# Kernel optimization log

Measured on AMD Instinct MI355X. Metric: run time of the kernel, lower is better.

Reference implementation:

```python
import jax, jax.numpy as jnp
import numpy as np

N_NODES = 100000
N_EDGES = 3200000
DROP_P = 0.5


def gcn_conv(x, W, b, src, dst, deg_inv_sqrt, n):
    # PyG GCNConv with self-loops already folded into (src, dst):
    # out[j] = sum_{(i->j)} dinv[i]*dinv[j] * (x W)[i] + b
    h = x @ W
    norm = deg_inv_sqrt[src] * deg_inv_sqrt[dst]          # [E+N]
    msg = h[src] * norm[:, None]                          # [E+N, d_out]
    out = jax.ops.segment_sum(msg, dst, num_segments=n)
    return out + b


def dropout(x, key, p=DROP_P):
    keep = jax.random.bernoulli(key, 1.0 - p, x.shape)
    return jnp.where(keep, x / (1.0 - p), 0.0)


def setup_inputs() -> dict:
    key = jax.random.key(0)
    ks = jax.random.split(key, 8)
    x = jax.random.normal(ks[0], (N_NODES, 64), dtype=jnp.float32)
    edge_index = jax.random.randint(ks[1], (2, N_EDGES), 0, N_NODES, dtype=jnp.int64)
    def glorot(k, fin, fout):
        lim = float(np.sqrt(6.0 / (fin + fout)))
        return jax.random.uniform(k, (fin, fout), jnp.float32, -lim, lim)
    return {
        "x": x,
        "edge_index": edge_index,
        "W1": glorot(ks[2], 64, 32), "b1": jnp.zeros((32,), jnp.float32),
        "W2": glorot(ks[3], 32, 64), "b2": jnp.zeros((64,), jnp.float32),
        "W3": glorot(ks[4], 64, 32), "b3": jnp.zeros((32,), jnp.float32),
    }


def reference(x, edge_index, W1, b1, W2, b2, W3, b3):
    n = x.shape[0]
    loops = jnp.arange(n, dtype=edge_index.dtype)
    src = jnp.concatenate([edge_index[0], loops])          # [E+N]
    dst = jnp.concatenate([edge_index[1], loops])
    deg = jax.ops.segment_sum(jnp.ones_like(dst, dtype=x.dtype), dst, num_segments=n)
    deg_inv_sqrt = jnp.where(deg > 0, jax.lax.rsqrt(deg), 0.0)

    dkey = jax.random.key(42)
    k1, k2 = jax.random.split(dkey)

    h = gcn_conv(x, W1, b1, src, dst, deg_inv_sqrt, n)
    h = jax.nn.celu(h)
    h = dropout(h, k1)
    h = gcn_conv(h, W2, b2, src, dst, deg_inv_sqrt, n)
    h = jax.nn.celu(h)
    h = dropout(h, k2)
    h = gcn_conv(h, W3, b3, src, dst, deg_inv_sqrt, n)
    return jax.nn.celu(h)
```

## Files before the change

kernel.cpp:

```cpp
#include <hip/hip_runtime.h>
#include <stdint.h>
#include <stddef.h>

typedef _Float16 half_t;
typedef _Float16 half4 __attribute__((ext_vector_type(4)));
typedef _Float16 half8 __attribute__((ext_vector_type(8)));

__host__ __device__ __forceinline__ uint32_t rotl32(uint32_t v, uint32_t r) {
  return (v << r) | (v >> (32u - r));
}

__host__ __device__ __forceinline__ void tf2x32(uint32_t k0, uint32_t k1,
                                                uint32_t x0, uint32_t x1,
                                                uint32_t& o0, uint32_t& o1) {
  uint32_t ks2 = k0 ^ k1 ^ 0x1BD11BDAu;
  x0 += k0; x1 += k1;
  x0 += x1; x1 = rotl32(x1, 13); x1 ^= x0;
  x0 += x1; x1 = rotl32(x1, 15); x1 ^= x0;
  x0 += x1; x1 = rotl32(x1, 26); x1 ^= x0;
  x0 += x1; x1 = rotl32(x1, 6);  x1 ^= x0;
  x0 += k1; x1 += ks2 + 1u;
  x0 += x1; x1 = rotl32(x1, 17); x1 ^= x0;
  x0 += x1; x1 = rotl32(x1, 29); x1 ^= x0;
  x0 += x1; x1 = rotl32(x1, 16); x1 ^= x0;
  x0 += x1; x1 = rotl32(x1, 24); x1 ^= x0;
  x0 += ks2; x1 += k0 + 2u;
  x0 += x1; x1 = rotl32(x1, 13); x1 ^= x0;
  x0 += x1; x1 = rotl32(x1, 15); x1 ^= x0;
  x0 += x1; x1 = rotl32(x1, 26); x1 ^= x0;
  x0 += x1; x1 = rotl32(x1, 6);  x1 ^= x0;
  x0 += k0; x1 += k1 + 3u;
  x0 += x1; x1 = rotl32(x1, 17); x1 ^= x0;
  x0 += x1; x1 = rotl32(x1, 29); x1 ^= x0;
  x0 += x1; x1 = rotl32(x1, 16); x1 ^= x0;
  x0 += x1; x1 = rotl32(x1, 24); x1 ^= x0;
  x0 += k1; x1 += ks2 + 4u;
  x0 += x1; x1 = rotl32(x1, 13); x1 ^= x0;
  x0 += x1; x1 = rotl32(x1, 15); x1 ^= x0;
  x0 += x1; x1 = rotl32(x1, 26); x1 ^= x0;
  x0 += x1; x1 = rotl32(x1, 6);  x1 ^= x0;
  x0 += ks2; x1 += k0 + 5u;
  o0 = x0; o1 = x1;
}

__device__ __forceinline__ bool tf_keep(uint32_t k0, uint32_t k1, uint32_t idx) {
  uint32_t o0, o1;
  tf2x32(k0, k1, 0u, idx, o0, o1);
  return ((o0 ^ o1) >> 31) == 0u;
}

#define CHUNK 4096
#define STASH 5120

__global__ __launch_bounds__(1024) void zero1024(uint32_t* __restrict__ p) {
  p[threadIdx.x] = 0u;
}

__global__ __launch_bounds__(1024) void k4_binhist(const int* __restrict__ src,
                                                   const int* __restrict__ dst,
                                                   uint32_t* __restrict__ tbl,
                                                   uint32_t* __restrict__ gbcnt,
                                                   uint32_t* __restrict__ staging,
                                                   int E, int NB) {
  __shared__ uint32_t lcur[1024];
  __shared__ uint32_t ls[1024];
  __shared__ uint32_t stage[CHUNK];
  int tid = threadIdx.x;
  lcur[tid] = 0u;
  __syncthreads();
  int base = blockIdx.x * CHUNK;
  int end = min(base + CHUNK, E);
  uint32_t dv[4], sv[4];
  int m = 0;
  for (int i = base + tid; i < end; i += 1024) {
    dv[m] = (uint32_t)dst[i];
    sv[m] = (uint32_t)src[i];
    ++m;
  }
  for (int q = 0; q < m; ++q) atomicAdd(&lcur[dv[q] >> 7], 1u);
  __syncthreads();
  uint32_t v = lcur[tid];
  ls[tid] = v;
  __syncthreads();
  for (int off = 1; off < 1024; off <<= 1) {
    uint32_t t = (tid >= off) ? ls[tid - off] : 0u;
    __syncthreads();
    if (tid >= off) ls[tid] += t;
    __syncthreads();
  }
  uint32_t excl = ls[tid] - v;
  if (tid < NB) {
    tbl[(size_t)blockIdx.x * NB + tid] = (excl << 16) | v;
    if (v) atomicAdd(&gbcnt[tid], v);
  }
  lcur[tid] = excl;
  __syncthreads();
  for (int q = 0; q < m; ++q) {
    uint32_t d = dv[q];
    uint32_t p = atomicAdd(&lcur[d >> 7], 1u);
    stage[p] = ((d & 127u) << 17) | sv[q];
  }
  __syncthreads();
  int cnt_total = end - base;
  uint32_t* outp = staging + (size_t)blockIdx.x * CHUNK;
  for (int i = tid; i < cnt_total; i += 1024) outp[i] = stage[i];
}

__global__ __launch_bounds__(1024) void k3_bscan(const uint32_t* __restrict__ gbcnt,
                                                 uint32_t* __restrict__ bbase, int NB) {
  __shared__ uint32_t s[1024];
  int i = threadIdx.x;
  uint32_t v = (i < NB) ? gbcnt[i] : 0u;
  s[i] = v;
  __syncthreads();
  for (int off = 1; off < 1024; off <<= 1) {
    uint32_t t = (i >= off) ? s[i - off] : 0u;
    __syncthreads();
    if (i >= off) s[i] += t;
    __syncthreads();
  }
  if (i < NB) bbase[i] = s[i] - v;
}

__global__ __launch_bounds__(1024) void k5_fin(
    const uint32_t* __restrict__ staging, const uint32_t* __restrict__ tbl,
    const uint32_t* __restrict__ bbase, uint32_t* __restrict__ rowp,
    float* __restrict__ dinv, uint32_t* __restrict__ esrc,
    int n, int E, int NBLK, int NB) {
  __shared__ uint32_t loff[1024];
  __shared__ uint32_t P[1025];
  __shared__ uint32_t ls[1024];
  __shared__ uint32_t stash[STASH];
  __shared__ uint32_t lc[128];
  __shared__ uint32_t sc[128];
  __shared__ uint32_t lcur[128];
  int tid = threadIdx.x;
  int b = blockIdx.x;
  if (tid < 128) lc[tid] = 0u;
  uint32_t packed = (tid < NBLK) ? tbl[(size_t)tid * NB + b] : 0u;
  uint32_t v = packed & 0xFFFFu;
  loff[tid] = packed >> 16;
  ls[tid] = v;
  __syncthreads();
  for (int off = 1; off < 1024; off <<= 1) {
    uint32_t t = (tid >= off) ? ls[tid - off] : 0u;
    __syncthreads();
    if (tid >= off) ls[tid] += t;
    __syncthreads();
  }
  P[tid] = ls[tid] - v;
  if (tid == 1023) P[1024] = ls[1023];
  __syncthreads();
  uint32_t total = P[NBLK];
  for (uint32_t q = (uint32_t)tid; q < total; q += 1024u) {
    int lo = 0, hi = NBLK;
    while (hi - lo > 1) {
      int mid = (lo + hi) >> 1;
      if (P[mid] <= q) lo = mid; else hi = mid;
    }
    uint32_t e = staging[(size_t)lo * CHUNK + loff[lo] + (q - P[lo])];
    if (q < (uint32_t)STASH) stash[q] = e;
    atomicAdd(&lc[e >> 17], 1u);
  }
  __syncthreads();
  uint32_t myc = (tid < 128) ? lc[tid] : 0u;
  if (tid < 128) sc[tid] = myc;
  __syncthreads();
  for (int off = 1; off < 128; off <<= 1) {
    uint32_t t = (tid < 128 && tid >= off) ? sc[tid - off] : 0u;
    __syncthreads();
    if (tid < 128 && tid >= off) sc[tid] += t;
    __syncthreads();
  }
  uint32_t s = bbase[b];
  if (tid < 128) {
    uint32_t gstart = s + sc[tid] - myc;
    int node = (b << 7) + tid;
    if (node < n) {
      rowp[node] = gstart;
      dinv[node] = 1.0f / sqrtf((float)(myc + 1u));
    }
    lcur[tid] = gstart;
  }
  if (b == 0 && tid == 0) rowp[n] = (uint32_t)E;
  __syncthreads();
  uint32_t lim = total < (uint32_t)STASH ? total : (uint32_t)STASH;
  for (uint32_t q = (uint32_t)tid; q < lim; q += 1024u) {
    uint32_t e = stash[q];
    uint32_t pos = atomicAdd(&lcur[e >> 17], 1u);
    esrc[pos] = e & 0x1FFFFu;
  }
  if (total > (uint32_t)STASH) {
    for (uint32_t q = (uint32_t)STASH + (uint32_t)tid; q < total; q += 1024u) {
      int lo = 0, hi = NBLK;
      while (hi - lo > 1) {
        int mid = (lo + hi) >> 1;
        if (P[mid] <= q) lo = mid; else hi = mid;
      }
      uint32_t e = staging[(size_t)lo * CHUNK + loff[lo] + (q - P[lo])];
      uint32_t pos = atomicAdd(&lcur[e >> 17], 1u);
      esrc[pos] = e & 0x1FFFFu;
    }
  }
}

__global__ __launch_bounds__(256) void gemm_n64_k32(
    const float* __restrict__ X, const float* __restrict__ W,
    const float* __restrict__ dinv, half_t* __restrict__ out16, int n) {
  __shared__ float Ws[64 * 32];
  __shared__ float Xs[32 * 68];
  int tid = threadIdx.x;
  {
    const float4* Wv = (const float4*)W;
    float4* Wsv = (float4*)Ws;
    Wsv[tid] = Wv[tid];
    Wsv[tid + 256] = Wv[tid + 256];
  }
  int row0 = blockIdx.x * 32;
  {
    const float4* Xv = (const float4*)(X + (size_t)row0 * 64);
    int lim = (n - row0) * 16;
    float4 z = make_float4(0.f, 0.f, 0.f, 0.f);
    int i0 = tid, i1 = tid + 256;
    float4 v0 = (i0 < lim) ? Xv[i0] : z;
    float4 v1 = (i1 < lim) ? Xv[i1] : z;
    *(float4*)(Xs + (i0 >> 4) * 68 + ((i0 & 15) << 2)) = v0;
    *(float4*)(Xs + (i1 >> 4) * 68 + ((i1 & 15) << 2)) = v1;
  }
  __syncthreads();
  int r = tid >> 3;
  int c4 = (tid & 7) << 2;
  int row = row0 + r;
  if (row >= n) return;
  float4 acc = make_float4(0.f, 0.f, 0.f, 0.f);
#pragma unroll
  for (int k = 0; k < 64; k += 4) {
    float4 xv = *(const float4*)(Xs + r * 68 + k);
    float4 w0 = *(const float4*)(Ws + (k + 0) * 32 + c4);
    float4 w1 = *(const float4*)(Ws + (k + 1) * 32 + c4);
    float4 w2 = *(const float4*)(Ws + (k + 2) * 32 + c4);
    float4 w3 = *(const float4*)(Ws + (k + 3) * 32 + c4);
    acc.x = fmaf(xv.x, w0.x, acc.x); acc.y = fmaf(xv.x, w0.y, acc.y);
    acc.z = fmaf(xv.x, w0.z, acc.z); acc.w = fmaf(xv.x, w0.w, acc.w);
    acc.x = fmaf(xv.y, w1.x, acc.x); acc.y = fmaf(xv.y, w1.y, acc.y);
    acc.z = fmaf(xv.y, w1.z, acc.z); acc.w = fmaf(xv.y, w1.w, acc.w);
    acc.x = fmaf(xv.z, w2.x, acc.x); acc.y = fmaf(xv.z, w2.y, acc.y);
    acc.z = fmaf(xv.z, w2.z, acc.z); acc.w = fmaf(xv.z, w2.w, acc.w);
    acc.x = fmaf(xv.w, w3.x, acc.x); acc.y = fmaf(xv.w, w3.y, acc.y);
    acc.z = fmaf(xv.w, w3.z, acc.z); acc.w = fmaf(xv.w, w3.w, acc.w);
  }
  float dj = dinv[row];
  half4 h;
  h.x = (half_t)(acc.x * dj); h.y = (half_t)(acc.y * dj);
  h.z = (half_t)(acc.z * dj); h.w = (half_t)(acc.w * dj);
  *(half4*)(out16 + (size_t)row * 32 + c4) = h;
}

__global__ __launch_bounds__(256) void gather_fin(
    const half_t* __restrict__ hs, const uint32_t* __restrict__ rowp,
    const uint32_t* __restrict__ esrc, const float* __restrict__ dinv,
    const float* __restrict__ bias, float* __restrict__ outf,
    half_t* __restrict__ outh, int n, int mode, uint32_t k0, uint32_t k1,
    float fone) {
  __shared__ __align__(16) float ldsred[256];
  (void)fone;
  int tid = threadIdx.x;
  int gt = blockIdx.x * 256 + tid;
  int j = gt >> 5;
  int g = tid >> 5;
  int l = tid & 31;
  int eslot = l >> 2;
  int chunk = l & 3;
  float acc[8] = {0.f, 0.f, 0.f, 0.f, 0.f, 0.f, 0.f, 0.f};
  uint32_t e0 = 0, deg = 0;
  float selfv = 0.f, dj = 0.f;
  if (j < n) {
    e0 = rowp[j];
    deg = rowp[j + 1] - e0;
    selfv = (float)hs[(size_t)j * 32 + l];
    dj = dinv[j];
  }
  const half_t* hp = hs + (size_t)(chunk << 3);
  const half8 hz = {(half_t)0, (half_t)0, (half_t)0, (half_t)0,
                    (half_t)0, (half_t)0, (half_t)0, (half_t)0};
  for (uint32_t base = 0; base < deg; base += 64u) {
    uint32_t rem = deg - base;
    if (rem > 64u) rem = 64u;
    uint32_t li0 = (uint32_t)l < rem ? (uint32_t)l : rem - 1u;
    uint32_t t1 = 32u + (uint32_t)l;
    uint32_t li1 = t1 < rem ? t1 : rem - 1u;
    uint32_t idx0 = __builtin_nontemporal_load(&esrc[e0 + base + li0]);
    uint32_t idx1 = __builtin_nontemporal_load(&esrc[e0 + base + li1]);
    half8 v0, v1, v2, v3, v4, v5, v6, v7;
#define GLOAD(KK, IDX, VOUT)                                              \
    {                                                                     \
      uint32_t kp = (uint32_t)(KK) + (uint32_t)eslot;                     \
      uint32_t s = (uint32_t)__shfl((int)(IDX), (int)(kp & 31u), 32);     \
      VOUT = hz;                                                          \
      if (kp < rem) VOUT = *(const half8*)(hp + ((size_t)s << 5));        \
    }
    GLOAD(0,  idx0, v0)
    GLOAD(8,  idx0, v1)
    GLOAD(16, idx0, v2)
    GLOAD(24, idx0, v3)
    GLOAD(32, idx1, v4)
    GLOAD(40, idx1, v5)
    GLOAD(48, idx1, v6)
    GLOAD(56, idx1, v7)
#undef GLOAD
    half8 s01 = v0 + v1;
    half8 s23 = v2 + v3;
    half8 s45 = v4 + v5;
    half8 s67 = v6 + v7;
#pragma unroll
    for (int q = 0; q < 8; ++q) {
      acc[q] += (float)s01[q];
      acc[q] += (float)s23[q];
      acc[q] += (float)s45[q];
      acc[q] += (float)s67[q];
    }
  }
#pragma unroll
  for (int m = 4; m <= 16; m <<= 1) {
#pragma unroll
    for (int q = 0; q < 8; ++q) acc[q] += __shfl_xor(acc[q], m);
  }
  if (l < 4) {
    *(float4*)(&ldsred[(g << 5) + (chunk << 3) + 0]) =
        make_float4(acc[0], acc[1], acc[2], acc[3]);
    *(float4*)(&ldsred[(g << 5) + (chunk << 3) + 4]) =
        make_float4(acc[4], acc[5], acc[6], acc[7]);
  }
  __builtin_amdgcn_wave_barrier();
  if (j >= n) return;
  float sum = ldsred[(g << 5) + l];
  sum += selfv;
  float v = dj * sum;
  if (mode == 1) {
    v += bias[l];
    v = v > 0.f ? v : expm1f(v);
    __builtin_nontemporal_store(v, &outf[gt]);
  } else if (mode == 3) {
    v += bias[l];
    v = v > 0.f ? v : expm1f(v);
    v = tf_keep(k0, k1, (uint32_t)gt) ? v * 2.f : 0.f;
    v *= dj;
    __builtin_nontemporal_store((half_t)v, &outh[gt]);
  } else {
    __builtin_nontemporal_store(v, &outf[gt]);
  }
}

__global__ __launch_bounds__(256) void gather_gemm2(
    const half_t* __restrict__ hs, const uint32_t* __restrict__ rowp,
    const uint32_t* __restrict__ esrc, const float* __restrict__ dinv,
    const float* __restrict__ W2, const float* __restrict__ b2,
    const float* __restrict__ W3, half_t* __restrict__ outh,
    int n, uint32_t k0, uint32_t k1) {
  __shared__ __align__(16) float ldsred[256];
  __shared__ __align__(16) float W2s[32 * 64];
  __shared__ __align__(16) float W3s[64 * 32];
  __shared__ __align__(16) float b2s[64];
  __shared__ __align__(16) float tls[8 * 64];
  int tid = threadIdx.x;
  {
    const float4* w2v = (const float4*)W2;
    const float4* w3v = (const float4*)W3;
    float4* s2 = (float4*)W2s;
    float4* s3 = (float4*)W3s;
    s2[tid] = w2v[tid];
    s2[tid + 256] = w2v[tid + 256];
    s3[tid] = w3v[tid];
    s3[tid + 256] = w3v[tid + 256];
    if (tid < 16) ((float4*)b2s)[tid] = ((const float4*)b2)[tid];
  }
  __syncthreads();
  int j = blockIdx.x * 8 + (tid >> 5);
  int g = tid >> 5;
  int l = tid & 31;
  int eslot = l >> 2;
  int chunk = l & 3;
  float acc[8] = {0.f, 0.f, 0.f, 0.f, 0.f, 0.f, 0.f, 0.f};
  uint32_t e0 = 0, deg = 0;
  float selfv = 0.f, dj = 0.f;
  if (j < n) {
    e0 = rowp[j];
    deg = rowp[j + 1] - e0;
    selfv = (float)hs[(size_t)j * 32 + l];
    dj = dinv[j];
  }
  const half_t* hp = hs + (size_t)(chunk << 3);
  const half8 hz = {(half_t)0, (half_t)0, (half_t)0, (half_t)0,
                    (half_t)0, (half_t)0, (half_t)0, (half_t)0};
  for (uint32_t base = 0; base < deg; base += 64u) {
    uint32_t rem = deg - base;
    if (rem > 64u) rem = 64u;
    uint32_t li0 = (uint32_t)l < rem ? (uint32_t)l : rem - 1u;
    uint32_t t1 = 32u + (uint32_t)l;
    uint32_t li1 = t1 < rem ? t1 : rem - 1u;
    uint32_t idx0 = __builtin_nontemporal_load(&esrc[e0 + base + li0]);
    uint32_t idx1 = __builtin_nontemporal_load(&esrc[e0 + base + li1]);
    half8 v0, v1, v2, v3, v4, v5, v6, v7;
#define GLOAD(KK, IDX, VOUT)                                              \
    {                                                                     \
      uint32_t kp = (uint32_t)(KK) + (uint32_t)eslot;                     \
      uint32_t s = (uint32_t)__shfl((int)(IDX), (int)(kp & 31u), 32);     \
      VOUT = hz;                                                          \
      if (kp < rem) VOUT = *(const half8*)(hp + ((size_t)s << 5));        \
    }
    GLOAD(0,  idx0, v0)
    GLOAD(8,  idx0, v1)
    GLOAD(16, idx0, v2)
    GLOAD(24, idx0, v3)
    GLOAD(32, idx1, v4)
    GLOAD(40, idx1, v5)
    GLOAD(48, idx1, v6)
    GLOAD(56, idx1, v7)
#undef GLOAD
    half8 s01 = v0 + v1;
    half8 s23 = v2 + v3;
    half8 s45 = v4 + v5;
    half8 s67 = v6 + v7;
#pragma unroll
    for (int q = 0; q < 8; ++q) {
      acc[q] += (float)s01[q];
      acc[q] += (float)s23[q];
      acc[q] += (float)s45[q];
      acc[q] += (float)s67[q];
    }
  }
#pragma unroll
  for (int m = 4; m <= 16; m <<= 1) {
#pragma unroll
    for (int q = 0; q < 8; ++q) acc[q] += __shfl_xor(acc[q], m);
  }
  if (l < 4) {
    *(float4*)(&ldsred[(g << 5) + (chunk << 3) + 0]) =
        make_float4(acc[0], acc[1], acc[2], acc[3]);
    *(float4*)(&ldsred[(g << 5) + (chunk << 3) + 4]) =
        make_float4(acc[4], acc[5], acc[6], acc[7]);
  }
  __builtin_amdgcn_wave_barrier();
  float hv = dj * (ldsred[(g << 5) + l] + selfv);
  __builtin_amdgcn_wave_barrier();
  ldsred[(g << 5) + l] = hv;
  __builtin_amdgcn_wave_barrier();
  int c0 = l << 1;
  float t0 = 0.f, t1v = 0.f;
#pragma unroll
  for (int k = 0; k < 32; ++k) {
    float xk = ldsred[(g << 5) + k];
    t0 = fmaf(xk, W2s[k * 64 + c0], t0);
    t1v = fmaf(xk, W2s[k * 64 + c0 + 1], t1v);
  }
  t0 += b2s[c0];
  t1v += b2s[c0 + 1];
  t0 = t0 > 0.f ? t0 : expm1f(t0);
  t1v = t1v > 0.f ? t1v : expm1f(t1v);
  uint32_t ridx = (uint32_t)j * 64u + (uint32_t)c0;
  t0 = tf_keep(k0, k1, ridx) ? t0 * 2.f : 0.f;
  t1v = tf_keep(k0, k1, ridx + 1u) ? t1v * 2.f : 0.f;
  tls[(g << 6) + c0] = t0;
  tls[(g << 6) + c0 + 1] = t1v;
  __builtin_amdgcn_wave_barrier();
  float a = 0.f;
#pragma unroll
  for (int c = 0; c < 64; ++c) {
    a = fmaf(tls[(g << 6) + c], W3s[c * 32 + l], a);
  }
  if (j < n) {
    __builtin_nontemporal_store((half_t)(a * dj), &outh[(size_t)j * 32 + l]);
  }
}

extern "C" void kernel_launch(void* const* d_in, const int* in_sizes, int n_in,
                              void* d_out, int out_size, void* d_ws, size_t ws_size,
                              hipStream_t stream) {
  const float* x  = (const float*)d_in[0];
  const int*   ei = (const int*)d_in[1];
  const float* W1 = (const float*)d_in[2];
  const float* b1 = (const float*)d_in[3];
  const float* W2 = (const float*)d_in[4];
  const float* b2 = (const float*)d_in[5];
  const float* W3 = (const float*)d_in[6];
  const float* b3 = (const float*)d_in[7];
  float* out = (float*)d_out;

  const int n = in_sizes[0] / 64;
  const int E = in_sizes[1] / 2;
  const int* src = ei;
  const int* dst = ei + E;

  char* ws = (char*)d_ws;
  size_t off = 0;
  auto alloc = [&](size_t bytes) {
    void* p = ws + off;
    off = (off + bytes + 255) & ~(size_t)255;
    return p;
  };
  const int NB   = (n + 127) >> 7;
  const int NBLK = (E + CHUNK - 1) / CHUNK;

  half_t*   A16   = (half_t*)alloc((size_t)n * 32 * 2);
  half_t*   B16   = (half_t*)alloc((size_t)n * 32 * 2);
  float*    dinv  = (float*)alloc((size_t)n * 4);
  uint32_t* rowp  = (uint32_t*)alloc((size_t)(n + 1) * 4);
  uint32_t* esrc  = (uint32_t*)alloc((size_t)E * 4);
  uint32_t* gbcnt = (uint32_t*)alloc(1024 * 4);
  uint32_t* bbase = (uint32_t*)alloc(1024 * 4);
  uint32_t* staging = (uint32_t*)alloc((size_t)NBLK * CHUNK * 4);
  uint32_t* tbl     = (uint32_t*)alloc((size_t)NBLK * NB * 4);
  (void)ws_size; (void)n_in; (void)out_size;

  uint32_t k1a, k1b, k2a, k2b;
  tf2x32(0u, 42u, 0u, 0u, k1a, k1b);
  tf2x32(0u, 42u, 0u, 1u, k2a, k2b);

  const int nv   = n * 32;
  const int gV   = (nv + 255) / 256;
  const int gG1  = (n + 31) / 32;
  dim3 blk(256);

  zero1024<<<1, dim3(1024), 0, stream>>>(gbcnt);
  k4_binhist<<<NBLK, dim3(1024), 0, stream>>>(src, dst, tbl, gbcnt, staging, E, NB);
  k3_bscan<<<1, dim3(1024), 0, stream>>>(gbcnt, bbase, NB);
  k5_fin<<<NB, dim3(1024), 0, stream>>>(staging, tbl, bbase, rowp, dinv, esrc, n, E, NBLK, NB);

  gemm_n64_k32<<<gG1, blk, 0, stream>>>(x, W1, dinv, A16, n);
  gather_fin<<<gV, blk, 0, stream>>>(A16, rowp, esrc, dinv, b1, nullptr, B16, n, 3, k1a, k1b, 1.0f);

  gather_gemm2<<<gV, blk, 0, stream>>>(B16, rowp, esrc, dinv, W2, b2, W3, A16, n, k2a, k2b);

  gather_fin<<<gV, blk, 0, stream>>>(A16, rowp, esrc, dinv, b3, out, nullptr, n, 1, 0u, 0u, 1.0f);
}
```

Before: 313.2 us.

## Fold bucket scan into k5_fin and transpose fused GEMM weights in LDS

Removes the separate single-block bucket-scan kernel: each k5_fin block now reduces the bucket counts of all preceding buckets itself to get its base offset. The fused gather_gemm2 kernel moves to 512-thread blocks (16 nodes per block) and stores W2/W3 transposed and padded in LDS so the per-node GEMMs can use float4 LDS reads. This cuts one launch and LDS traffic in the small matmuls, at the cost of redundant per-block reductions and a larger LDS footprint per block, which may lower occupancy.

```diff
diff --git a/kernel.cpp b/kernel.cpp
--- a/kernel.cpp
+++ b/kernel.cpp
@@ -106,25 +106,9 @@
   for (int i = tid; i < cnt_total; i += 1024) outp[i] = stage[i];
 }
 
-__global__ __launch_bounds__(1024) void k3_bscan(const uint32_t* __restrict__ gbcnt,
-                                                 uint32_t* __restrict__ bbase, int NB) {
-  __shared__ uint32_t s[1024];
-  int i = threadIdx.x;
-  uint32_t v = (i < NB) ? gbcnt[i] : 0u;
-  s[i] = v;
-  __syncthreads();
-  for (int off = 1; off < 1024; off <<= 1) {
-    uint32_t t = (i >= off) ? s[i - off] : 0u;
-    __syncthreads();
-    if (i >= off) s[i] += t;
-    __syncthreads();
-  }
-  if (i < NB) bbase[i] = s[i] - v;
-}
-
 __global__ __launch_bounds__(1024) void k5_fin(
     const uint32_t* __restrict__ staging, const uint32_t* __restrict__ tbl,
-    const uint32_t* __restrict__ bbase, uint32_t* __restrict__ rowp,
+    const uint32_t* __restrict__ gbcnt, uint32_t* __restrict__ rowp,
     float* __restrict__ dinv, uint32_t* __restrict__ esrc,
     int n, int E, int NBLK, int NB) {
   __shared__ uint32_t loff[1024];
@@ -152,6 +136,14 @@
   if (tid == 1023) P[1024] = ls[1023];
   __syncthreads();
   uint32_t total = P[NBLK];
+  ls[tid] = (tid < b) ? gbcnt[tid] : 0u;
+  __syncthreads();
+  for (int off = 512; off > 0; off >>= 1) {
+    if (tid < off) ls[tid] += ls[tid + off];
+    __syncthreads();
+  }
+  uint32_t sbase = ls[0];
+  __syncthreads();
   for (uint32_t q = (uint32_t)tid; q < total; q += 1024u) {
     int lo = 0, hi = NBLK;
     while (hi - lo > 1) {
@@ -172,9 +164,8 @@
     if (tid < 128 && tid >= off) sc[tid] += t;
     __syncthreads();
   }
-  uint32_t s = bbase[b];
   if (tid < 128) {
-    uint32_t gstart = s + sc[tid] - myc;
+    uint32_t gstart = sbase + sc[tid] - myc;
     int node = (b << 7) + tid;
     if (node < n) {
       rowp[node] = gstart;
@@ -351,33 +342,29 @@
   }
 }
 
-__global__ __launch_bounds__(256) void gather_gemm2(
+__global__ __launch_bounds__(512) void gather_gemm2(
     const half_t* __restrict__ hs, const uint32_t* __restrict__ rowp,
     const uint32_t* __restrict__ esrc, const float* __restrict__ dinv,
     const float* __restrict__ W2, const float* __restrict__ b2,
     const float* __restrict__ W3, half_t* __restrict__ outh,
     int n, uint32_t k0, uint32_t k1) {
-  __shared__ __align__(16) float ldsred[256];
-  __shared__ __align__(16) float W2s[32 * 64];
-  __shared__ __align__(16) float W3s[64 * 32];
+  __shared__ __align__(16) float ldsred[512];
+  __shared__ __align__(16) float W2t[64 * 36];
+  __shared__ __align__(16) float W3t[32 * 68];
+  __shared__ __align__(16) float tls[16 * 64];
   __shared__ __align__(16) float b2s[64];
-  __shared__ __align__(16) float tls[8 * 64];
   int tid = threadIdx.x;
-  {
-    const float4* w2v = (const float4*)W2;
-    const float4* w3v = (const float4*)W3;
-    float4* s2 = (float4*)W2s;
-    float4* s3 = (float4*)W3s;
-    s2[tid] = w2v[tid];
-    s2[tid + 256] = w2v[tid + 256];
-    s3[tid] = w3v[tid];
-    s3[tid + 256] = w3v[tid + 256];
-    if (tid < 16) ((float4*)b2s)[tid] = ((const float4*)b2)[tid];
-  }
-  __syncthreads();
-  int j = blockIdx.x * 8 + (tid >> 5);
+  for (int i = tid; i < 2048; i += 512) {
+    float w2v = W2[i];
+    W2t[(i & 63) * 36 + (i >> 6)] = w2v;
+    float w3v = W3[i];
+    W3t[(i & 31) * 68 + (i >> 5)] = w3v;
+  }
+  if (tid < 64) b2s[tid] = b2[tid];
+  __syncthreads();
   int g = tid >> 5;
   int l = tid & 31;
+  int j = blockIdx.x * 16 + g;
   int eslot = l >> 2;
   int chunk = l & 3;
   float acc[8] = {0.f, 0.f, 0.f, 0.f, 0.f, 0.f, 0.f, 0.f};
@@ -445,28 +432,34 @@
   __builtin_amdgcn_wave_barrier();
   ldsred[(g << 5) + l] = hv;
   __builtin_amdgcn_wave_barrier();
-  int c0 = l << 1;
-  float t0 = 0.f, t1v = 0.f;
-#pragma unroll
-  for (int k = 0; k < 32; ++k) {
-    float xk = ldsred[(g << 5) + k];
-    t0 = fmaf(xk, W2s[k * 64 + c0], t0);
-    t1v = fmaf(xk, W2s[k * 64 + c0 + 1], t1v);
-  }
-  t0 += b2s[c0];
-  t1v += b2s[c0 + 1];
-  t0 = t0 > 0.f ? t0 : expm1f(t0);
-  t1v = t1v > 0.f ? t1v : expm1f(t1v);
-  uint32_t ridx = (uint32_t)j * 64u + (uint32_t)c0;
-  t0 = tf_keep(k0, k1, ridx) ? t0 * 2.f : 0.f;
-  t1v = tf_keep(k0, k1, ridx + 1u) ? t1v * 2.f : 0.f;
-  tls[(g << 6) + c0] = t0;
-  tls[(g << 6) + c0 + 1] = t1v;
+  float ta = 0.f, tb = 0.f;
+#pragma unroll
+  for (int k = 0; k < 32; k += 4) {
+    float4 hv4 = *(const float4*)(&ldsred[(g << 5) + k]);
+    float4 wa = *(const float4*)(&W2t[l * 36 + k]);
+    float4 wb = *(const float4*)(&W2t[(l + 32) * 36 + k]);
+    ta = fmaf(hv4.x, wa.x, ta); ta = fmaf(hv4.y, wa.y, ta);
+    ta = fmaf(hv4.z, wa.z, ta); ta = fmaf(hv4.w, wa.w, ta);
+    tb = fmaf(hv4.x, wb.x, tb); tb = fmaf(hv4.y, wb.y, tb);
+    tb = fmaf(hv4.z, wb.z, tb); tb = fmaf(hv4.w, wb.w, tb);
+  }
+  ta += b2s[l];
+  tb += b2s[l + 32];
+  ta = ta > 0.f ? ta : expm1f(ta);
+  tb = tb > 0.f ? tb : expm1f(tb);
+  uint32_t ridx = (uint32_t)j * 64u + (uint32_t)l;
+  ta = tf_keep(k0, k1, ridx) ? ta * 2.f : 0.f;
+  tb = tf_keep(k0, k1, ridx + 32u) ? tb * 2.f : 0.f;
+  tls[(g << 6) + l] = ta;
+  tls[(g << 6) + l + 32] = tb;
   __builtin_amdgcn_wave_barrier();
   float a = 0.f;
 #pragma unroll
-  for (int c = 0; c < 64; ++c) {
-    a = fmaf(tls[(g << 6) + c], W3s[c * 32 + l], a);
+  for (int c = 0; c < 64; c += 4) {
+    float4 tv = *(const float4*)(&tls[(g << 6) + c]);
+    float4 wv = *(const float4*)(&W3t[l * 68 + c]);
+    a = fmaf(tv.x, wv.x, a); a = fmaf(tv.y, wv.y, a);
+    a = fmaf(tv.z, wv.z, a); a = fmaf(tv.w, wv.w, a);
   }
   if (j < n) {
     __builtin_nontemporal_store((half_t)(a * dj), &outh[(size_t)j * 32 + l]);
@@ -507,7 +500,6 @@
   uint32_t* rowp  = (uint32_t*)alloc((size_t)(n + 1) * 4);
   uint32_t* esrc  = (uint32_t*)alloc((size_t)E * 4);
   uint32_t* gbcnt = (uint32_t*)alloc(1024 * 4);
-  uint32_t* bbase = (uint32_t*)alloc(1024 * 4);
   uint32_t* staging = (uint32_t*)alloc((size_t)NBLK * CHUNK * 4);
   uint32_t* tbl     = (uint32_t*)alloc((size_t)NBLK * NB * 4);
   (void)ws_size; (void)n_in; (void)out_size;
@@ -519,17 +511,17 @@
   const int nv   = n * 32;
   const int gV   = (nv + 255) / 256;
   const int gG1  = (n + 31) / 32;
+  const int gGF  = (n + 15) / 16;
   dim3 blk(256);
 
   zero1024<<<1, dim3(1024), 0, stream>>>(gbcnt);
   k4_binhist<<<NBLK, dim3(1024), 0, stream>>>(src, dst, tbl, gbcnt, staging, E, NB);
-  k3_bscan<<<1, dim3(1024), 0, stream>>>(gbcnt, bbase, NB);
-  k5_fin<<<NB, dim3(1024), 0, stream>>>(staging, tbl, bbase, rowp, dinv, esrc, n, E, NBLK, NB);
+  k5_fin<<<NB, dim3(1024), 0, stream>>>(staging, tbl, gbcnt, rowp, dinv, esrc, n, E, NBLK, NB);
 
   gemm_n64_k32<<<gG1, blk, 0, stream>>>(x, W1, dinv, A16, n);
   gather_fin<<<gV, blk, 0, stream>>>(A16, rowp, esrc, dinv, b1, nullptr, B16, n, 3, k1a, k1b, 1.0f);
 
-  gather_gemm2<<<gV, blk, 0, stream>>>(B16, rowp, esrc, dinv, W2, b2, W3, A16, n, k2a, k2b);
+  gather_gemm2<<<gGF, dim3(512), 0, stream>>>(B16, rowp, esrc, dinv, W2, b2, W3, A16, n, k2a, k2b);
 
   gather_fin<<<gV, blk, 0, stream>>>(A16, rowp, esrc, dinv, b3, out, nullptr, n, 1, 0u, 0u, 1.0f);
 }
```

Measured after the change: 316.7 us. About the same (+1.1%).

## Split each gather into two source-range passes for cache locality

Applied to the files above, without the earlier changes.

Each aggregation now runs as two passes. The first gathers only neighbours with source index below n/2 and writes float partial sums to a workspace buffer. The second gathers the upper half, adds the partials and applies the epilogue. The aim is to keep the gathered feature half (about 3.2MB fp16) resident in cache and cut random DRAM traffic. In exchange it adds extra launches, re-reads the edge lists twice, and writes and reads a 12.8MB float partial buffer per layer.

```diff
diff --git a/kernel.cpp b/kernel.cpp
--- a/kernel.cpp
+++ b/kernel.cpp
@@ -260,13 +260,129 @@
     const half_t* __restrict__ hs, const uint32_t* __restrict__ rowp,
     const uint32_t* __restrict__ esrc, const float* __restrict__ dinv,
     const float* __restrict__ bias, float* __restrict__ outf,
-    half_t* __restrict__ outh, int n, int mode, uint32_t k0, uint32_t k1,
-    float fone) {
+    half_t* __restrict__ outh, float* __restrict__ part,
+    int n, int nh, int phase, int mode, uint32_t k0, uint32_t k1) {
   __shared__ __align__(16) float ldsred[256];
-  (void)fone;
   int tid = threadIdx.x;
   int gt = blockIdx.x * 256 + tid;
   int j = gt >> 5;
+  int g = tid >> 5;
+  int l = tid & 31;
+  int eslot = l >> 2;
+  int chunk = l & 3;
+  float acc[8] = {0.f, 0.f, 0.f, 0.f, 0.f, 0.f, 0.f, 0.f};
+  uint32_t e0 = 0, deg = 0;
+  float selfv = 0.f, dj = 0.f;
+  if (j < n) {
+    e0 = rowp[j];
+    deg = rowp[j + 1] - e0;
+    if (phase == 1) {
+      selfv = (float)hs[(size_t)j * 32 + l];
+      dj = dinv[j];
+    }
+  }
+  const half_t* hp = hs + (size_t)(chunk << 3);
+  const half8 hz = {(half_t)0, (half_t)0, (half_t)0, (half_t)0,
+                    (half_t)0, (half_t)0, (half_t)0, (half_t)0};
+  for (uint32_t base = 0; base < deg; base += 64u) {
+    uint32_t rem = deg - base;
+    if (rem > 64u) rem = 64u;
+    uint32_t li0 = (uint32_t)l < rem ? (uint32_t)l : rem - 1u;
+    uint32_t t1 = 32u + (uint32_t)l;
+    uint32_t li1 = t1 < rem ? t1 : rem - 1u;
+    uint32_t idx0 = __builtin_nontemporal_load(&esrc[e0 + base + li0]);
+    uint32_t idx1 = __builtin_nontemporal_load(&esrc[e0 + base + li1]);
+    half8 v0, v1, v2, v3, v4, v5, v6, v7;
+#define GLOAD(KK, IDX, VOUT)                                              \
+    {                                                                     \
+      uint32_t kp = (uint32_t)(KK) + (uint32_t)eslot;                     \
+      uint32_t s = (uint32_t)__shfl((int)(IDX), (int)(kp & 31u), 32);     \
+      bool sel = phase ? (s >= (uint32_t)nh) : (s < (uint32_t)nh);        \
+      VOUT = hz;                                                          \
+      if (kp < rem && sel) VOUT = *(const half8*)(hp + ((size_t)s << 5)); \
+    }
+    GLOAD(0,  idx0, v0)
+    GLOAD(8,  idx0, v1)
+    GLOAD(16, idx0, v2)
+    GLOAD(24, idx0, v3)
+    GLOAD(32, idx1, v4)
+    GLOAD(40, idx1, v5)
+    GLOAD(48, idx1, v6)
+    GLOAD(56, idx1, v7)
+#undef GLOAD
+    half8 s01 = v0 + v1;
+    half8 s23 = v2 + v3;
+    half8 s45 = v4 + v5;
+    half8 s67 = v6 + v7;
+#pragma unroll
+    for (int q = 0; q < 8; ++q) {
+      acc[q] += (float)s01[q];
+      acc[q] += (float)s23[q];
+      acc[q] += (float)s45[q];
+      acc[q] += (float)s67[q];
+    }
+  }
+#pragma unroll
+  for (int m = 4; m <= 16; m <<= 1) {
+#pragma unroll
+    for (int q = 0; q < 8; ++q) acc[q] += __shfl_xor(acc[q], m);
+  }
+  if (l < 4) {
+    *(float4*)(&ldsred[(g << 5) + (chunk << 3) + 0]) =
+        make_float4(acc[0], acc[1], acc[2], acc[3]);
+    *(float4*)(&ldsred[(g << 5) + (chunk << 3) + 4]) =
+        make_float4(acc[4], acc[5], acc[6], acc[7]);
+  }
+  __builtin_amdgcn_wave_barrier();
+  if (j >= n) return;
+  float sum = ldsred[(g << 5) + l];
+  if (phase == 0) {
+    __builtin_nontemporal_store(sum, &part[gt]);
+    return;
+  }
+  sum += __builtin_nontemporal_load(&part[gt]);
+  sum += selfv;
+  float v = dj * sum;
+  if (mode == 1) {
+    v += bias[l];
+    v = v > 0.f ? v : expm1f(v);
+    __builtin_nontemporal_store(v, &outf[gt]);
+  } else if (mode == 3) {
+    v += bias[l];
+    v = v > 0.f ? v : expm1f(v);
+    v = tf_keep(k0, k1, (uint32_t)gt) ? v * 2.f : 0.f;
+    v *= dj;
+    __builtin_nontemporal_store((half_t)v, &outh[gt]);
+  } else {
+    __builtin_nontemporal_store(v, &outf[gt]);
+  }
+}
+
+__global__ __launch_bounds__(256) void gather_gemm2(
+    const half_t* __restrict__ hs, const uint32_t* __restrict__ rowp,
+    const uint32_t* __restrict__ esrc, const float* __restrict__ dinv,
+    const float* __restrict__ W2, const float* __restrict__ b2,
+    const float* __restrict__ W3, half_t* __restrict__ outh,
+    const float* __restrict__ part, int n, int nh, uint32_t k0, uint32_t k1) {
+  __shared__ __align__(16) float ldsred[256];
+  __shared__ __align__(16) float W2s[32 * 64];
+  __shared__ __align__(16) float W3s[64 * 32];
+  __shared__ __align__(16) float b2s[64];
+  __shared__ __align__(16) float tls[8 * 64];
+  int tid = threadIdx.x;
+  {
+    const float4* w2v = (const float4*)W2;
+    const float4* w3v = (const float4*)W3;
+    float4* s2 = (float4*)W2s;
+    float4* s3 = (float4*)W3s;
+    s2[tid] = w2v[tid];
+    s2[tid + 256] = w2v[tid + 256];
+    s3[tid] = w3v[tid];
+    s3[tid + 256] = w3v[tid + 256];
+    if (tid < 16) ((float4*)b2s)[tid] = ((const float4*)b2)[tid];
+  }
+  __syncthreads();
+  int j = blockIdx.x * 8 + (tid >> 5);
   int g = tid >> 5;
   int l = tid & 31;
   int eslot = l >> 2;
@@ -297,7 +413,8 @@
       uint32_t kp = (uint32_t)(KK) + (uint32_t)eslot;                     \
       uint32_t s = (uint32_t)__shfl((int)(IDX), (int)(kp & 31u), 32);     \
       VOUT = hz;                                                          \
-      if (kp < rem) VOUT = *(const half8*)(hp + ((size_t)s << 5));        \
+      if (kp < rem && s >= (uint32_t)nh)                                  \
+        VOUT = *(const half8*)(hp + ((size_t)s << 5));                    \
     }
     GLOAD(0,  idx0, v0)
     GLOAD(8,  idx0, v1)
@@ -332,116 +449,8 @@
         make_float4(acc[4], acc[5], acc[6], acc[7]);
   }
   __builtin_amdgcn_wave_barrier();
-  if (j >= n) return;
-  float sum = ldsred[(g << 5) + l];
-  sum += selfv;
-  float v = dj * sum;
-  if (mode == 1) {
-    v += bias[l];
-    v = v > 0.f ? v : expm1f(v);
-    __builtin_nontemporal_store(v, &outf[gt]);
-  } else if (mode == 3) {
-    v += bias[l];
-    v = v > 0.f ? v : expm1f(v);
-    v = tf_keep(k0, k1, (uint32_t)gt) ? v * 2.f : 0.f;
-    v *= dj;
-    __builtin_nontemporal_store((half_t)v, &outh[gt]);
-  } else {
-    __builtin_nontemporal_store(v, &outf[gt]);
-  }
-}
-
-__global__ __launch_bounds__(256) void gather_gemm2(
-    const half_t* __restrict__ hs, const uint32_t* __restrict__ rowp,
-    const uint32_t* __restrict__ esrc, const float* __restrict__ dinv,
-    const float* __restrict__ W2, const float* __restrict__ b2,
-    const float* __restrict__ W3, half_t* __restrict__ outh,
-    int n, uint32_t k0, uint32_t k1) {
-  __shared__ __align__(16) float ldsred[256];
-  __shared__ __align__(16) float W2s[32 * 64];
-  __shared__ __align__(16) float W3s[64 * 32];
-  __shared__ __align__(16) float b2s[64];
-  __shared__ __align__(16) float tls[8 * 64];
-  int tid = threadIdx.x;
-  {
-    const float4* w2v = (const float4*)W2;
-    const float4* w3v = (const float4*)W3;
-    float4* s2 = (float4*)W2s;
-    float4* s3 = (float4*)W3s;
-    s2[tid] = w2v[tid];
-    s2[tid + 256] = w2v[tid + 256];
-    s3[tid] = w3v[tid];
-    s3[tid + 256] = w3v[tid + 256];
-    if (tid < 16) ((float4*)b2s)[tid] = ((const float4*)b2)[tid];
-  }
-  __syncthreads();
-  int j = blockIdx.x * 8 + (tid >> 5);
-  int g = tid >> 5;
-  int l = tid & 31;
-  int eslot = l >> 2;
-  int chunk = l & 3;
-  float acc[8] = {0.f, 0.f, 0.f, 0.f, 0.f, 0.f, 0.f, 0.f};
-  uint32_t e0 = 0, deg = 0;
-  float selfv = 0.f, dj = 0.f;
-  if (j < n) {
-    e0 = rowp[j];
-    deg = rowp[j + 1] - e0;
-    selfv = (float)hs[(size_t)j * 32 + l];
-    dj = dinv[j];
-  }
-  const half_t* hp = hs + (size_t)(chunk << 3);
-  const half8 hz = {(half_t)0, (half_t)0, (half_t)0, (half_t)0,
-                    (half_t)0, (half_t)0, (half_t)0, (half_t)0};
-  for (uint32_t base = 0; base < deg; base += 64u) {
-    uint32_t rem = deg - base;
-    if (rem > 64u) rem = 64u;
-    uint32_t li0 = (uint32_t)l < rem ? (uint32_t)l : rem - 1u;
-    uint32_t t1 = 32u + (uint32_t)l;
-    uint32_t li1 = t1 < rem ? t1 : rem - 1u;
-    uint32_t idx0 = __builtin_nontemporal_load(&esrc[e0 + base + li0]);
-    uint32_t idx1 = __builtin_nontemporal_load(&esrc[e0 + base + li1]);
-    half8 v0, v1, v2, v3, v4, v5, v6, v7;
-#define GLOAD(KK, IDX, VOUT)                                              \
-    {                                                                     \
-      uint32_t kp = (uint32_t)(KK) + (uint32_t)eslot;                     \
-      uint32_t s = (uint32_t)__shfl((int)(IDX), (int)(kp & 31u), 32);     \
-      VOUT = hz;                                                          \
-      if (kp < rem) VOUT = *(const half8*)(hp + ((size_t)s << 5));        \
-    }
-    GLOAD(0,  idx0, v0)
-    GLOAD(8,  idx0, v1)
-    GLOAD(16, idx0, v2)
-    GLOAD(24, idx0, v3)
-    GLOAD(32, idx1, v4)
-    GLOAD(40, idx1, v5)
-    GLOAD(48, idx1, v6)
-    GLOAD(56, idx1, v7)
-#undef GLOAD
-    half8 s01 = v0 + v1;
-    half8 s23 = v2 + v3;
-    half8 s45 = v4 + v5;
-    half8 s67 = v6 + v7;
-#pragma unroll
-    for (int q = 0; q < 8; ++q) {
-      acc[q] += (float)s01[q];
-      acc[q] += (float)s23[q];
-      acc[q] += (float)s45[q];
-      acc[q] += (float)s67[q];
-    }
-  }
-#pragma unroll
-  for (int m = 4; m <= 16; m <<= 1) {
-#pragma unroll
-    for (int q = 0; q < 8; ++q) acc[q] += __shfl_xor(acc[q], m);
-  }
-  if (l < 4) {
-    *(float4*)(&ldsred[(g << 5) + (chunk << 3) + 0]) =
-        make_float4(acc[0], acc[1], acc[2], acc[3]);
-    *(float4*)(&ldsred[(g << 5) + (chunk << 3) + 4]) =
-        make_float4(acc[4], acc[5], acc[6], acc[7]);
-  }
-  __builtin_amdgcn_wave_barrier();
-  float hv = dj * (ldsred[(g << 5) + l] + selfv);
+  float pv = (j < n) ? __builtin_nontemporal_load(&part[(size_t)j * 32 + l]) : 0.f;
+  float hv = dj * (ldsred[(g << 5) + l] + pv + selfv);
   __builtin_amdgcn_wave_barrier();
   ldsred[(g << 5) + l] = hv;
   __builtin_amdgcn_wave_barrier();
@@ -488,6 +497,7 @@
 
   const int n = in_sizes[0] / 64;
   const int E = in_sizes[1] / 2;
+  const int nh = (n + 1) >> 1;
   const int* src = ei;
   const int* dst = ei + E;
 
@@ -503,6 +513,7 @@
 
   half_t*   A16   = (half_t*)alloc((size_t)n * 32 * 2);
   half_t*   B16   = (half_t*)alloc((size_t)n * 32 * 2);
+  float*    part  = (float*)alloc((size_t)n * 32 * 4);
   float*    dinv  = (float*)alloc((size_t)n * 4);
   uint32_t* rowp  = (uint32_t*)alloc((size_t)(n + 1) * 4);
   uint32_t* esrc  = (uint32_t*)alloc((size_t)E * 4);
@@ -527,9 +538,12 @@
   k5_fin<<<NB, dim3(1024), 0, stream>>>(staging, tbl, bbase, rowp, dinv, esrc, n, E, NBLK, NB);
 
   gemm_n64_k32<<<gG1, blk, 0, stream>>>(x, W1, dinv, A16, n);
-  gather_fin<<<gV, blk, 0, stream>>>(A16, rowp, esrc, dinv, b1, nullptr, B16, n, 3, k1a, k1b, 1.0f);
-
-  gather_gemm2<<<gV, blk, 0, stream>>>(B16, rowp, esrc, dinv, W2, b2, W3, A16, n, k2a, k2b);
-
-  gather_fin<<<gV, blk, 0, stream>>>(A16, rowp, esrc, dinv, b3, out, nullptr, n, 1, 0u, 0u, 1.0f);
-}
+  gather_fin<<<gV, blk, 0, stream>>>(A16, rowp, esrc, dinv, b1, nullptr, B16, part, n, nh, 0, 3, k1a, k1b);
+  gather_fin<<<gV, blk, 0, stream>>>(A16, rowp, esrc, dinv, b1, nullptr, B16, part, n, nh, 1, 3, k1a, k1b);
+
+  gather_fin<<<gV, blk, 0, stream>>>(B16, rowp, esrc, dinv, nullptr, nullptr, nullptr, part, n, nh, 0, 0, 0u, 0u);
+  gather_gemm2<<<gV, blk, 0, stream>>>(B16, rowp, esrc, dinv, W2, b2, W3, A16, part, n, nh, k2a, k2b);
+
+  gather_fin<<<gV, blk, 0, stream>>>(A16, rowp, esrc, dinv, b3, out, nullptr, part, n, nh, 0, 1, 0u, 0u);
+  gather_fin<<<gV, blk, 0, stream>>>(A16, rowp, esrc, dinv, b3, out, nullptr, part, n, nh, 1, 1, 0u, 0u);
+}
```

Result: slower. 409.9 us (+30.9%).
